# Optimization experiments

Measured on AMD Instinct MI355X. Metric: run time of the kernel, lower is better.

Reference implementation:

```python
import jax, jax.numpy as jnp
import numpy as np

EPS = 1e-20

def setup_inputs() -> dict:
    key = jax.random.key(0)
    k1, k2, k3, k4 = jax.random.split(key, 4)
    B, C, H, W, K = 8, 64, 512, 512, 16
    hex_list = ["0x1a1c2c", "0x5d275d", "0xb13e53", "0xef7d57", "0xffcd75", "0xa7f070",
                "0x38b764", "0x257179", "0x29366f", "0x3b5dc9", "0x41a6f6", "0x73eff7",
                "0xf4f4f4", "0x94b0c2", "0x566c86", "0x333c57"]
    rgb = np.array([[int(h[2:][i:i+2], 16) for i in (0, 2, 4)] for h in hex_list],
                   dtype=np.float32) / 255.0
    return {
        "x": jax.random.normal(k1, (B, C, H, W), dtype=jnp.float32),
        "conv_w": jax.random.normal(k2, (K, C), dtype=jnp.float32) * (1.0 / np.sqrt(C)),
        "conv_b": jax.random.normal(k3, (K,), dtype=jnp.float32) * 0.01,
        "palette": jnp.asarray(rgb),                      # [K, 3], fixed constant
        "unif": jax.random.uniform(k4, (B, H, W, K), dtype=jnp.float32),
    }

def reference(x, conv_w, conv_b, palette, unif):
    # 1x1 conv == per-pixel matmul over channel dim: [B,C,H,W] x [K,C] -> [B,K,H,W]
    logits = jnp.einsum('bchw,kc->bkhw', x, conv_w) + conv_b[None, :, None, None]
    color_prob = jax.nn.softmax(logits, axis=1)           # [B,K,H,W]
    # weighted sum over palette: sum_k prob[b,k,h,w] * palette[k,c]
    blended = jnp.einsum('bkhw,kc->bchw', color_prob, palette)  # [B,3,H,W]
    # multinomial sample via Gumbel-max over K (same distribution as torch.multinomial)
    logp = jax.nn.log_softmax(logits, axis=1).transpose(0, 2, 3, 1)  # [B,H,W,K]
    gumbel = -jnp.log(-jnp.log(unif + EPS) + EPS)
    idx = jnp.argmax(logp + gumbel, axis=-1)              # [B,H,W] int
    discrete = palette[idx].transpose(0, 3, 1, 2)         # [B,3,H,W]
    # straight-through estimator
    pixel_art = jax.lax.stop_gradient(discrete - blended) + blended
    return pixel_art
```

## Files before the change

kernel.cpp:

```cpp
#include <hip/hip_runtime.h>
#include <math.h>

#define HW_ (512 * 512)
#define C_ 64
#define K_ 16
#define B_ 8
#define TOTAL_ (B_ * HW_)

__global__ __launch_bounds__(256) void transpose_w_kernel(const float* __restrict__ w,
                                                          float* __restrict__ wt) {
    int i = blockIdx.x * blockDim.x + threadIdx.x;
    if (i < K_ * C_) {
        int k = i >> 6;
        int c = i & 63;
        wt[c * K_ + k] = w[i];
    }
}

__device__ __forceinline__ void epilogue(const float* acc, const float4* up4,
                                         const float* __restrict__ palette,
                                         float& cr, float& cg, float& cb) {
    float m = acc[0];
    #pragma unroll
    for (int k = 1; k < K_; ++k) m = fmaxf(m, acc[k]);
    float s = 0.0f;
    #pragma unroll
    for (int k = 0; k < K_; ++k) s += expf(acc[k] - m);
    float ls = logf(s);

    float best = -INFINITY;
    int bi = 0;
    #pragma unroll
    for (int q = 0; q < 4; ++q) {
        float4 v = up4[q];
        float g0 = -logf(-logf(v.x + 1e-20f) + 1e-20f);
        float g1 = -logf(-logf(v.y + 1e-20f) + 1e-20f);
        float g2 = -logf(-logf(v.z + 1e-20f) + 1e-20f);
        float g3 = -logf(-logf(v.w + 1e-20f) + 1e-20f);
        float t0 = (acc[q * 4 + 0] - m) - ls + g0;
        float t1 = (acc[q * 4 + 1] - m) - ls + g1;
        float t2 = (acc[q * 4 + 2] - m) - ls + g2;
        float t3 = (acc[q * 4 + 3] - m) - ls + g3;
        if (t0 > best) { best = t0; bi = q * 4 + 0; }
        if (t1 > best) { best = t1; bi = q * 4 + 1; }
        if (t2 > best) { best = t2; bi = q * 4 + 2; }
        if (t3 > best) { best = t3; bi = q * 4 + 3; }
    }
    cr = palette[bi * 3 + 0];
    cg = palette[bi * 3 + 1];
    cb = palette[bi * 3 + 2];
}

__global__ __launch_bounds__(256, 8) void quantizer_kernel(
    const float* __restrict__ x,
    const float* __restrict__ wt,
    const float* __restrict__ bias,
    const float* __restrict__ palette,
    const float* __restrict__ unif,
    float* __restrict__ out)
{
    int tid = blockIdx.x * blockDim.x + threadIdx.x;

    #pragma unroll 1
    for (int p = tid; p < TOTAL_; p += 524288) {
        int b = p >> 18;
        int hw = p & (HW_ - 1);
        const float* xp = x + (size_t)b * C_ * HW_ + (size_t)hw;

        float acc[K_];
        #pragma unroll
        for (int k = 0; k < K_; ++k) acc[k] = bias[k];

        float cur[8], nxt[8];
        #pragma unroll
        for (int i = 0; i < 8; ++i) cur[i] = xp[(size_t)i * HW_];

        #pragma unroll 1
        for (int g = 0; g < 8; ++g) {
            int c0 = g * 8;
            if (g < 7) {
                #pragma unroll
                for (int i = 0; i < 8; ++i)
                    nxt[i] = xp[(size_t)(c0 + 8 + i) * HW_];
            }
            const float* wp = wt + c0 * K_;
            #pragma unroll
            for (int k = 0; k < K_; ++k) {
                float a = acc[k];
                #pragma unroll
                for (int i = 0; i < 8; ++i)
                    a = fmaf(cur[i], wp[i * K_ + k], a);
                acc[k] = a;
            }
            #pragma unroll
            for (int i = 0; i < 8; ++i) cur[i] = nxt[i];
        }

        const float4* up4 = reinterpret_cast<const float4*>(unif + (size_t)p * K_);
        float cr, cg, cb;
        epilogue(acc, up4, palette, cr, cg, cb);

        size_t obase = (size_t)b * 3 * HW_ + (size_t)hw;
        out[obase]                   = cr;
        out[obase + (size_t)HW_]     = cg;
        out[obase + 2 * (size_t)HW_] = cb;
    }
}

extern "C" void kernel_launch(void* const* d_in, const int* in_sizes, int n_in,
                              void* d_out, int out_size, void* d_ws, size_t ws_size,
                              hipStream_t stream) {
    const float* x       = (const float*)d_in[0];
    const float* conv_w  = (const float*)d_in[1];
    const float* conv_b  = (const float*)d_in[2];
    const float* palette = (const float*)d_in[3];
    const float* unif    = (const float*)d_in[4];
    float* out = (float*)d_out;
    float* wt  = (float*)d_ws;

    hipLaunchKernelGGL(transpose_w_kernel, dim3(4), dim3(256), 0, stream, conv_w, wt);

    hipLaunchKernelGGL(quantizer_kernel, dim3(2048), dim3(256), 0, stream,
                       x, wt, conv_b, palette, unif, out);
}
```

Before: 149.7 us.

## Stream x tiles into LDS with double-buffered async global_load_lds

Replaces the per-thread register prefetch of x channels with direct global-to-LDS async loads (global_load_lds, 16 bytes per lane), double-buffered over 16-channel tiles with vmcnt waits and barriers. Each block now owns 256 pixels across 4 batch images and prefetches the next image's first tile during the last group. The goal is more memory-level parallelism and less register pressure so HBM streaming of x overlaps the FMA work. In exchange it adds two barriers per tile and hand-counted vmcnt waits that must match the number of outstanding loads; the unif loads in the epilogue are also counted by vmcnt.

```diff
diff --git a/kernel.cpp b/kernel.cpp
--- a/kernel.cpp
+++ b/kernel.cpp
@@ -5,7 +5,6 @@
 #define C_ 64
 #define K_ 16
 #define B_ 8
-#define TOTAL_ (B_ * HW_)
 
 __global__ __launch_bounds__(256) void transpose_w_kernel(const float* __restrict__ w,
                                                           float* __restrict__ wt) {
@@ -15,6 +14,22 @@
         int c = i & 63;
         wt[c * K_ + k] = w[i];
     }
+}
+
+__device__ __forceinline__ void gl_lds16(const float* g, float* l) {
+    __builtin_amdgcn_global_load_lds(
+        (const __attribute__((address_space(1))) void*)g,
+        (__attribute__((address_space(3))) void*)l,
+        16, 0, 0);
+}
+
+__device__ __forceinline__ void issue_tile(const float* __restrict__ x, float* ldsbuf,
+                                           int b, int cbase, int hw0, int wid, int lane) {
+    const float* gp = x + (size_t)(b * C_ + cbase + wid * 4) * HW_ + hw0 + 4 * lane;
+    float* lp = ldsbuf + (wid * 4) * 256 + 4 * lane;
+    #pragma unroll
+    for (int i = 0; i < 4; ++i)
+        gl_lds16(gp + (size_t)i * HW_, lp + i * 256);
 }
 
 __device__ __forceinline__ void epilogue(const float* acc, const float4* up4,
@@ -59,48 +74,56 @@
     const float* __restrict__ unif,
     float* __restrict__ out)
 {
-    int tid = blockIdx.x * blockDim.x + threadIdx.x;
+    __shared__ float lds[2][16 * 256];
+
+    const int t = threadIdx.x;
+    const int wid = t >> 6;
+    const int lane = t & 63;
+    const int blk = blockIdx.x;
+    const int b0 = blk >> 10;
+    const int hw0 = (blk & 1023) * 256;
+
+    issue_tile(x, lds[0], b0, 0, hw0, wid, lane);
 
     #pragma unroll 1
-    for (int p = tid; p < TOTAL_; p += 524288) {
-        int b = p >> 18;
-        int hw = p & (HW_ - 1);
-        const float* xp = x + (size_t)b * C_ * HW_ + (size_t)hw;
+    for (int r = 0; r < 4; ++r) {
+        const int b = b0 + 2 * r;
 
         float acc[K_];
         #pragma unroll
         for (int k = 0; k < K_; ++k) acc[k] = bias[k];
 
-        float cur[8], nxt[8];
         #pragma unroll
-        for (int i = 0; i < 8; ++i) cur[i] = xp[(size_t)i * HW_];
+        for (int g = 0; g < 4; ++g) {
+            if (g < 3) {
+                issue_tile(x, lds[(g + 1) & 1], b, (g + 1) * 16, hw0, wid, lane);
+                asm volatile("s_waitcnt vmcnt(4)" ::: "memory");
+            } else if (r < 3) {
+                issue_tile(x, lds[0], b0 + 2 * (r + 1), 0, hw0, wid, lane);
+                asm volatile("s_waitcnt vmcnt(4)" ::: "memory");
+            } else {
+                asm volatile("s_waitcnt vmcnt(0)" ::: "memory");
+            }
+            __builtin_amdgcn_s_barrier();
 
-        #pragma unroll 1
-        for (int g = 0; g < 8; ++g) {
-            int c0 = g * 8;
-            if (g < 7) {
+            const float* buf = lds[g & 1];
+            const float* wp = wt + (g * 16) * K_;
+            #pragma unroll
+            for (int cl = 0; cl < 16; ++cl) {
+                float xv = buf[cl * 256 + t];
                 #pragma unroll
-                for (int i = 0; i < 8; ++i)
-                    nxt[i] = xp[(size_t)(c0 + 8 + i) * HW_];
+                for (int k = 0; k < K_; ++k)
+                    acc[k] = fmaf(xv, wp[cl * K_ + k], acc[k]);
             }
-            const float* wp = wt + c0 * K_;
-            #pragma unroll
-            for (int k = 0; k < K_; ++k) {
-                float a = acc[k];
-                #pragma unroll
-                for (int i = 0; i < 8; ++i)
-                    a = fmaf(cur[i], wp[i * K_ + k], a);
-                acc[k] = a;
-            }
-            #pragma unroll
-            for (int i = 0; i < 8; ++i) cur[i] = nxt[i];
+            __builtin_amdgcn_s_barrier();
         }
 
-        const float4* up4 = reinterpret_cast<const float4*>(unif + (size_t)p * K_);
+        size_t p = (size_t)b * HW_ + (size_t)(hw0 + t);
+        const float4* up4 = reinterpret_cast<const float4*>(unif + p * K_);
         float cr, cg, cb;
         epilogue(acc, up4, palette, cr, cg, cb);
 
-        size_t obase = (size_t)b * 3 * HW_ + (size_t)hw;
+        size_t obase = (size_t)b * 3 * HW_ + (size_t)(hw0 + t);
         out[obase]                   = cr;
         out[obase + (size_t)HW_]     = cg;
         out[obase + 2 * (size_t)HW_] = cb;
```

Measured after the change: 210.1 us. 1.4x slower.
